# Performance work log

Hardware: AMD Instinct MI355X
Metric: run time of the kernel (lower is better)

The kernel has to match this reference:

```python
import jax, jax.numpy as jnp
import numpy as np

D_MODEL = 768
N_HEADS = 4
HEAD_DIM = D_MODEL // N_HEADS


def setup_inputs() -> dict:
    key = jax.random.key(0)
    ks = jax.random.split(key, 9)
    B, S = 4, 2048
    scale = 1.0 / np.sqrt(D_MODEL)
    inputs = jax.random.normal(ks[0], (B, S, D_MODEL), dtype=jnp.float32)
    # Linear weights stored as [in, out] for x @ W + b
    Wq = jax.random.normal(ks[1], (D_MODEL, D_MODEL), dtype=jnp.float32) * scale
    bq = jnp.zeros((D_MODEL,), dtype=jnp.float32)
    Wk = jax.random.normal(ks[2], (D_MODEL, D_MODEL), dtype=jnp.float32) * scale
    bk = jnp.zeros((D_MODEL,), dtype=jnp.float32)
    Wv = jax.random.normal(ks[3], (D_MODEL, D_MODEL), dtype=jnp.float32) * scale
    bv = jnp.zeros((D_MODEL,), dtype=jnp.float32)
    Wo = jax.random.normal(ks[4], (D_MODEL, D_MODEL), dtype=jnp.float32) * scale
    bo = jnp.zeros((D_MODEL,), dtype=jnp.float32)
    return {"inputs": inputs, "Wq": Wq, "bq": bq, "Wk": Wk, "bk": bk,
            "Wv": Wv, "bv": bv, "Wo": Wo, "bo": bo}


def reference(inputs, Wq, bq, Wk, bk, Wv, bv, Wo, bo):
    B, S, _ = inputs.shape
    H, Dh = N_HEADS, HEAD_DIM
    # projections -> [B, H, S, Dh]
    def split_heads(x):
        return x.reshape(B, S, H, Dh).transpose(0, 2, 1, 3)
    Q = split_heads(inputs @ Wq + bq)
    K = split_heads(inputs @ Wk + bk)
    V = split_heads(inputs @ Wv + bv)
    scores = jnp.einsum('bhqd,bhkd->bhqk', Q, K) / jnp.sqrt(jnp.float32(Dh))
    causal = jnp.tril(jnp.ones((S, S), dtype=bool))  # True = keep
    scores = jnp.where(causal, scores, -jnp.inf)
    weights = jax.nn.softmax(scores, axis=-1)
    # dropout is identity in eval mode
    ctx = jnp.einsum('bhqk,bhkd->bhqd', weights, V)
    ctx = ctx.transpose(0, 2, 1, 3).reshape(B, S, H * Dh)
    return ctx @ Wo + bo
```

## Files before the change

### kernel.cpp

```cpp
#include <hip/hip_runtime.h>
#include <hip/hip_bf16.h>
#include <cstddef>

typedef __attribute__((ext_vector_type(8))) short short8;
typedef __attribute__((ext_vector_type(4))) float f32x4;
typedef __attribute__((ext_vector_type(16))) float f32x16;
typedef __attribute__((ext_vector_type(4))) unsigned short u16x4;

#define D_MODEL 768
#define N_HEADS 4
#define HEAD_DIM 192
#define BATCH 4
#define SEQ 2048
#define M_ROWS (BATCH*SEQ)
#define QSCALE 0.10411754f

__device__ __forceinline__ short f2bf(float f) {
  union { float f; unsigned u; } v; v.f = f;
  unsigned r = v.u + 0x7FFFu + ((v.u >> 16) & 1u);
  return (short)(r >> 16);
}

__device__ __forceinline__ float fexp2(float x) {
  return __builtin_amdgcn_exp2f(x);
}

__device__ __forceinline__ void gl_lds16(const void* g, void* l) {
  __builtin_amdgcn_global_load_lds(
      (const __attribute__((address_space(1))) void*)g,
      (__attribute__((address_space(3))) void*)l, 16, 0, 0);
}

__global__ __launch_bounds__(256) void cast_kernel(const float* __restrict__ src,
                                                   short* __restrict__ dst, int n8) {
  int i = blockIdx.x * 256 + threadIdx.x;
  if (i >= n8) return;
  const float4* s = (const float4*)src;
  float4 a = s[2 * i], b = s[2 * i + 1];
  short8 o;
  o[0] = f2bf(a.x); o[1] = f2bf(a.y); o[2] = f2bf(a.z); o[3] = f2bf(a.w);
  o[4] = f2bf(b.x); o[5] = f2bf(b.y); o[6] = f2bf(b.z); o[7] = f2bf(b.w);
  *(short8*)(dst + (size_t)i * 8) = o;
}

__global__ __launch_bounds__(256) void wtrans4(const float* __restrict__ W0,
                                               const float* __restrict__ W1,
                                               const float* __restrict__ W2,
                                               const float* __restrict__ W3,
                                               short* __restrict__ Wqkvt,
                                               short* __restrict__ Wot) {
  __shared__ float tile[32][33];
  int z = blockIdx.z;
  const float* W = z == 0 ? W0 : (z == 1 ? W1 : (z == 2 ? W2 : W3));
  short* Wt = z < 3 ? (Wqkvt + (size_t)z * 768 * 768) : Wot;
  int k0 = blockIdx.x * 32, n0 = blockIdx.y * 32;
  int tc = threadIdx.x & 31, tr = threadIdx.x >> 5;
#pragma unroll
  for (int i = 0; i < 4; i++)
    tile[tr + i * 8][tc] = W[(size_t)(k0 + tr + i * 8) * D_MODEL + n0 + tc];
  __syncthreads();
#pragma unroll
  for (int i = 0; i < 4; i++)
    Wt[(size_t)(n0 + tr + i * 8) * D_MODEL + k0 + tc] = f2bf(tile[tc][tr + i * 8]);
}

template <int MODE>
__global__ __launch_bounds__(256, 4) void gemm_bf16(const short* __restrict__ A,
                                                    const short* __restrict__ Wt,
                                                    const float* __restrict__ b0,
                                                    const float* __restrict__ b1,
                                                    const float* __restrict__ b2,
                                                    short* __restrict__ oQ,
                                                    short* __restrict__ oK,
                                                    short* __restrict__ oV,
                                                    float* __restrict__ oF,
                                                    int N, int NB) {
  __shared__ short As[128 * 64];
  __shared__ short Bs[128 * 64];
  const int K = 768;
  const int lid = blockIdx.x;
  const int nlid = (lid & 7) * ((int)gridDim.x >> 3) + (lid >> 3);
  const int m0 = (nlid / NB) * 128, n0 = (nlid % NB) * 128;
  const int t = threadIdx.x, lane = t & 63, w = t >> 6;
  const int wr = w >> 1, wc = w & 1, lr = lane & 15, lg = lane >> 4;

  f32x4 acc[4][4] = {};

  for (int k0 = 0; k0 < K; k0 += 64) {
#pragma unroll
    for (int i = 0; i < 4; i++) {
      int id = w * 4 + i;
      int row = id * 8 + (lane >> 3);
      int cc = (lane & 7) ^ (row & 7);
      gl_lds16(A + (size_t)(m0 + row) * K + k0 + cc * 8, As + id * 512);
      gl_lds16(Wt + (size_t)(n0 + row) * K + k0 + cc * 8, Bs + id * 512);
    }
    __syncthreads();
#pragma unroll
    for (int kb = 0; kb < 2; kb++) {
      short8 a[4], b[4];
#pragma unroll
      for (int m = 0; m < 4; m++) {
        int row = wr * 64 + m * 16 + lr;
        a[m] = *(const short8*)&As[row * 64 + (((kb * 4 + lg) ^ (row & 7)) << 3)];
      }
#pragma unroll
      for (int n = 0; n < 4; n++) {
        int row = wc * 64 + n * 16 + lr;
        b[n] = *(const short8*)&Bs[row * 64 + (((kb * 4 + lg) ^ (row & 7)) << 3)];
      }
#pragma unroll
      for (int m = 0; m < 4; m++)
#pragma unroll
        for (int n = 0; n < 4; n++)
          acc[m][n] = __builtin_amdgcn_mfma_f32_16x16x32_bf16(a[m], b[n], acc[m][n], 0, 0, 0);
    }
    __syncthreads();
  }

  if (MODE == 0) {
#pragma unroll
    for (int m = 0; m < 4; m++)
#pragma unroll
      for (int n = 0; n < 4; n++) {
        int col = n0 + wc * 64 + n * 16 + lr;
        float bv = b0[col];
#pragma unroll
        for (int r = 0; r < 4; r++) {
          int row = m0 + wr * 64 + m * 16 + lg * 4 + r;
          oF[(size_t)row * N + col] = acc[m][n][r] + bv;
        }
      }
  } else {
    const int bb = m0 >> 11;
#pragma unroll
    for (int m = 0; m < 4; m++) {
      int s0 = (m0 & (SEQ - 1)) + wr * 64 + m * 16 + lg * 4;
#pragma unroll
      for (int n = 0; n < 4; n++) {
        int col = n0 + wc * 64 + n * 16 + lr;
        int seg = col / 768;
        int d = col - seg * 768;
        int h = d / HEAD_DIM, dd = d - h * HEAD_DIM;
        int bh = bb * N_HEADS + h;
        float bv = (seg == 0 ? b0 : (seg == 1 ? b1 : b2))[d];
        if (seg < 2) {
          short* dst = seg == 0 ? oQ : oK;
          float qs = seg == 0 ? QSCALE : 1.0f;
#pragma unroll
          for (int r = 0; r < 4; r++)
            dst[((size_t)bh * SEQ + s0 + r) * HEAD_DIM + dd] = f2bf((acc[m][n][r] + bv) * qs);
        } else {
          u16x4 pk;
#pragma unroll
          for (int r = 0; r < 4; r++) pk[r] = (unsigned short)f2bf(acc[m][n][r] + bv);
          *(u16x4*)&oV[((size_t)bh * HEAD_DIM + dd) * SEQ + s0] = pk;
        }
      }
    }
  }
}

__device__ __forceinline__ void stage_kv(const short* Kp, const short* Vp, int kbase,
                                         short* KsB, short* VsB, int w, int lane) {
#pragma unroll
  for (int i = 0; i < 6; i++) {
    int id = w * 6 + i;
    int o16 = id * 64 + lane;
    int row = o16 / 24, cc0 = o16 - row * 24;
    int cc = cc0 ^ (row & 7);
    gl_lds16(Kp + (size_t)(kbase + row) * HEAD_DIM + cc * 8, KsB + id * 512);
  }
#pragma unroll
  for (int i = 0; i < 6; i++) {
    int id = w * 6 + i;
    int o16 = id * 64 + lane;
    int row = o16 >> 3, cc = (o16 & 7) ^ (row & 7);
    gl_lds16(Vp + (size_t)row * SEQ + kbase + cc * 8, VsB + id * 512);
  }
}

__global__ __launch_bounds__(256, 2) void attn_kernel(const short* __restrict__ Q,
                                                      const short* __restrict__ Kg,
                                                      const short* __restrict__ Vt,
                                                      short* __restrict__ ctx) {
  __shared__ short smem[64 * 192 + 192 * 64];
  __shared__ float mlbuf[128];
  short* Ks = smem;
  short* Vs = smem + 64 * 192;
  float* obuf = (float*)smem;

  const int i = blockIdx.x;
  int bh, qt;
  if (i < 256) { bh = i & 15; qt = 31 - (i >> 4); }
  else         { int j = i - 256; bh = j & 15; qt = j >> 4; }

  const int b = bh >> 2, head = bh & 3;
  const short* Qp = Q + (size_t)bh * SEQ * HEAD_DIM;
  const short* Kp = Kg + (size_t)bh * SEQ * HEAD_DIM;
  const short* Vp = Vt + (size_t)bh * HEAD_DIM * SEQ;
  const int t = threadIdx.x, lane = t & 63, w = t >> 6;
  const int wq = w >> 1, wk = w & 1;
  const int l31 = lane & 31, hl = lane >> 5;

  const int nkb = qt + 1;
  const int q0w = qt * 64 + wq * 32;
  const int qlane = q0w + l31;

  short8 qf[12];
#pragma unroll
  for (int c = 0; c < 12; c++)
    qf[c] = *(const short8*)&Qp[(size_t)qlane * HEAD_DIM + c * 16 + hl * 8];

  f32x16 oacc[6];
#pragma unroll
  for (int d = 0; d < 6; d++) oacc[d] = 0.f;
  float m = -3.0e38f, lsum = 0.f;

  for (int kb = 0; kb < nkb; kb++) {
    const int kbase = kb * 64;
    stage_kv(Kp, Vp, kbase, Ks, Vs, w, lane);
    asm volatile("s_waitcnt vmcnt(0)" ::: "memory");
    __builtin_amdgcn_s_barrier();
    asm volatile("" ::: "memory");

    if (kbase + wk * 32 <= q0w + 31) {
      f32x16 sacc = 0.f, sacc2 = 0.f;
      const int krow = wk * 32 + l31;
      const int krb = krow * 192;
      const int kswz = (krow & 7) << 3;
      __builtin_amdgcn_s_setprio(1);
#pragma unroll
      for (int c = 0; c < 12; c += 2) {
        short8 kf0 = *(const short8*)&Ks[krb + ((c * 16 + hl * 8) ^ kswz)];
        short8 kf1 = *(const short8*)&Ks[krb + (((c + 1) * 16 + hl * 8) ^ kswz)];
        sacc = __builtin_amdgcn_mfma_f32_32x32x16_bf16(kf0, qf[c], sacc, 0, 0, 0);
        sacc2 = __builtin_amdgcn_mfma_f32_32x32x16_bf16(kf1, qf[c + 1], sacc2, 0, 0, 0);
      }
      __builtin_amdgcn_s_setprio(0);

      float sv[16];
      const bool need_mask = (kbase + wk * 32 + 31) > q0w;
      const int kb0 = kbase + wk * 32 + 4 * hl;
#pragma unroll
      for (int r = 0; r < 16; r++) {
        float v = sacc[r] + sacc2[r];
        if (need_mask) {
          int kg = kb0 + (r & 3) + 8 * (r >> 2);
          if (kg > qlane) v = -3.0e38f;
        }
        sv[r] = v;
      }
      float ma = fmaxf(fmaxf(sv[0], sv[1]), fmaxf(sv[2], sv[3]));
      float mb = fmaxf(fmaxf(sv[4], sv[5]), fmaxf(sv[6], sv[7]));
      float mc = fmaxf(fmaxf(sv[8], sv[9]), fmaxf(sv[10], sv[11]));
      float md = fmaxf(fmaxf(sv[12], sv[13]), fmaxf(sv[14], sv[15]));
      float mx = fmaxf(fmaxf(ma, mb), fmaxf(mc, md));
      mx = fmaxf(mx, __shfl_xor(mx, 32, 64));
      if (!__all(mx <= m + 8.0f)) {
        float mn = fmaxf(m, mx);
        float al = fexp2(m - mn);
        m = mn;
        lsum *= al;
#pragma unroll
        for (int d = 0; d < 6; d++) oacc[d] *= al;
      }
      float pr[16];
#pragma unroll
      for (int r = 0; r < 16; r++) pr[r] = fexp2(sv[r] - m);
      float sa = (pr[0] + pr[1]) + (pr[2] + pr[3]);
      float sb = (pr[4] + pr[5]) + (pr[6] + pr[7]);
      float sc = (pr[8] + pr[9]) + (pr[10] + pr[11]);
      float sd = (pr[12] + pr[13]) + (pr[14] + pr[15]);
      float rs = (sa + sb) + (sc + sd);
      rs += __shfl_xor(rs, 32, 64);
      lsum += rs;

      unsigned pk[8], ex[8];
#pragma unroll
      for (int j = 0; j < 8; j++) {
        unsigned r0;
        asm("v_cvt_pk_bf16_f32 %0, %1, %2" : "=v"(r0) : "v"(pr[2 * j]), "v"(pr[2 * j + 1]));
        pk[j] = r0;
      }
#pragma unroll
      for (int j = 0; j < 8; j++) ex[j] = __shfl_xor((int)pk[j], 32, 64);
      union { unsigned u[4]; short8 s8; } f0, f1;
      f0.u[0] = hl ? ex[2] : pk[0];
      f0.u[1] = hl ? ex[3] : pk[1];
      f0.u[2] = hl ? pk[2] : ex[0];
      f0.u[3] = hl ? pk[3] : ex[1];
      f1.u[0] = hl ? ex[6] : pk[4];
      f1.u[1] = hl ? ex[7] : pk[5];
      f1.u[2] = hl ? pk[6] : ex[4];
      f1.u[3] = hl ? pk[7] : ex[5];

      __builtin_amdgcn_s_setprio(1);
#pragma unroll
      for (int db = 0; db < 6; db++) {
        const int vrow = db * 32 + l31;
        const int vrb = vrow * 64;
        const int vswz = (vrow & 7) << 3;
        short8 va = *(const short8*)&Vs[vrb + ((wk * 32 + hl * 8) ^ vswz)];
        oacc[db] = __builtin_amdgcn_mfma_f32_32x32x16_bf16(va, f0.s8, oacc[db], 0, 0, 0);
        short8 vb = *(const short8*)&Vs[vrb + ((wk * 32 + 16 + hl * 8) ^ vswz)];
        oacc[db] = __builtin_amdgcn_mfma_f32_32x32x16_bf16(vb, f1.s8, oacc[db], 0, 0, 0);
      }
      __builtin_amdgcn_s_setprio(0);
    }
    asm volatile("" ::: "memory");
    __builtin_amdgcn_s_barrier();
  }

  __syncthreads();
  if (wk == 1) {
    if (lane < 32) {
      mlbuf[wq * 64 + lane] = m;
      mlbuf[wq * 64 + 32 + lane] = lsum;
    }
#pragma unroll
    for (int db = 0; db < 6; db++)
#pragma unroll
      for (int g = 0; g < 4; g++) {
        int d = db * 32 + 8 * g + 4 * hl;
        f32x4 vv;
        vv[0] = oacc[db][4 * g];
        vv[1] = oacc[db][4 * g + 1];
        vv[2] = oacc[db][4 * g + 2];
        vv[3] = oacc[db][4 * g + 3];
        *(f32x4*)&obuf[(wq * 32 + l31) * 192 + (d ^ ((l31 & 7) << 2))] = vv;
      }
  }
  __syncthreads();
  if (wk == 0) {
    float m1 = mlbuf[wq * 64 + l31];
    float l1 = mlbuf[wq * 64 + 32 + l31];
    float ms = fmaxf(m, m1);
    float a0 = fexp2(m - ms), a1 = fexp2(m1 - ms);
    float lt = lsum * a0 + l1 * a1;
    float rl = 1.0f / lt;
#pragma unroll
    for (int db = 0; db < 6; db++)
#pragma unroll
      for (int g = 0; g < 4; g++) {
        int d = db * 32 + 8 * g + 4 * hl;
        f32x4 rd = *(const f32x4*)&obuf[(wq * 32 + l31) * 192 + (d ^ ((l31 & 7) << 2))];
        u16x4 pkk;
#pragma unroll
        for (int r2 = 0; r2 < 4; r2++) {
          float v = (oacc[db][4 * g + r2] * a0 + rd[r2] * a1) * rl;
          pkk[r2] = (unsigned short)f2bf(v);
        }
        *(u16x4*)&ctx[((size_t)b * SEQ + qlane) * D_MODEL + head * HEAD_DIM + d] = pkk;
      }
  }
}

extern "C" void kernel_launch(void* const* d_in, const int* in_sizes, int n_in,
                              void* d_out, int out_size, void* d_ws, size_t ws_size,
                              hipStream_t stream) {
  const float* X  = (const float*)d_in[0];
  const float* Wq = (const float*)d_in[1];
  const float* bq = (const float*)d_in[2];
  const float* Wk = (const float*)d_in[3];
  const float* bk = (const float*)d_in[4];
  const float* Wv = (const float*)d_in[5];
  const float* bv = (const float*)d_in[6];
  const float* Wo = (const float*)d_in[7];
  const float* bo = (const float*)d_in[8];

  char* ws = (char*)d_ws;
  const size_t XB = (size_t)M_ROWS * D_MODEL * 2;
  const size_t WQKV = (size_t)3 * D_MODEL * D_MODEL * 2;
  const size_t WB = (size_t)D_MODEL * D_MODEL * 2;

  short* Xb    = (short*)(ws);
  short* Wqkvt = (short*)(ws + XB);
  short* Wot   = (short*)(ws + XB + WQKV);
  short* Qb    = (short*)(ws + XB + WQKV + WB + 12288);
  short* Kb    = (short*)(ws + XB + WQKV + WB + 12288 + XB);
  short* Vtb   = (short*)(ws + XB + WQKV + WB + 12288 + 2 * XB);
  short* Cb    = (short*)(ws + XB + WQKV + WB + 12288 + 3 * XB);

  const int n8x = M_ROWS * D_MODEL / 8;
  cast_kernel<<<(n8x + 255) / 256, 256, 0, stream>>>(X, Xb, n8x);
  wtrans4<<<dim3(24, 24, 4), 256, 0, stream>>>(Wq, Wk, Wv, Wo, Wqkvt, Wot);

  gemm_bf16<1><<<1152, 256, 0, stream>>>(Xb, Wqkvt, bq, bk, bv,
                                         Qb, Kb, Vtb, nullptr, 2304, 18);

  attn_kernel<<<512, 256, 0, stream>>>(Qb, Kb, Vtb, Cb);

  gemm_bf16<0><<<384, 256, 0, stream>>>(Cb, Wot, bo, bo, bo,
                                        nullptr, nullptr, nullptr, (float*)d_out, 768, 6);
}
```

Before: 141.5 us.

## Split causal attention KV range across two blocks and merge partials in separate kernel

Attention now uses 128-row query tiles with each warp owning 32 query rows, and splits each tile's KV range into two halves handled by separate blocks. Each block writes fp32 partial outputs plus max and sum to workspace, and a new merge kernel combines them into bf16 context. This replaces the old in-block split of key columns across warps, which needed an LDS reduction and did redundant Q loads. The aim is better load balance and more K/V reuse per stage. The cost is an extra kernel launch and about 50 MB of fp32 partial traffic through global memory.

```diff
diff --git a/kernel.cpp b/kernel.cpp
--- a/kernel.cpp
+++ b/kernel.cpp
@@ -183,28 +183,27 @@
 __global__ __launch_bounds__(256, 2) void attn_kernel(const short* __restrict__ Q,
                                                       const short* __restrict__ Kg,
                                                       const short* __restrict__ Vt,
-                                                      short* __restrict__ ctx) {
+                                                      float* __restrict__ Pbuf,
+                                                      float* __restrict__ Mbuf) {
   __shared__ short smem[64 * 192 + 192 * 64];
-  __shared__ float mlbuf[128];
   short* Ks = smem;
   short* Vs = smem + 64 * 192;
-  float* obuf = (float*)smem;
 
   const int i = blockIdx.x;
-  int bh, qt;
-  if (i < 256) { bh = i & 15; qt = 31 - (i >> 4); }
-  else         { int j = i - 256; bh = j & 15; qt = j >> 4; }
-
-  const int b = bh >> 2, head = bh & 3;
+  int bh, j, h;
+  if (i < 256) { bh = i & 15; j = i >> 4;        h = 0; }
+  else         { int p = i - 256; bh = p & 15; j = 15 - (p >> 4); h = 1; }
+  const int u0 = h == 0 ? 0 : j + 1;
+  const int u1 = h == 0 ? j + 1 : 2 * j + 2;
+  const int sidx = (bh * 16 + j) * 2 + h;
+
   const short* Qp = Q + (size_t)bh * SEQ * HEAD_DIM;
   const short* Kp = Kg + (size_t)bh * SEQ * HEAD_DIM;
   const short* Vp = Vt + (size_t)bh * HEAD_DIM * SEQ;
   const int t = threadIdx.x, lane = t & 63, w = t >> 6;
-  const int wq = w >> 1, wk = w & 1;
   const int l31 = lane & 31, hl = lane >> 5;
 
-  const int nkb = qt + 1;
-  const int q0w = qt * 64 + wq * 32;
+  const int q0w = j * 128 + w * 32;
   const int qlane = q0w + l31;
 
   short8 qf[12];
@@ -217,142 +216,151 @@
   for (int d = 0; d < 6; d++) oacc[d] = 0.f;
   float m = -3.0e38f, lsum = 0.f;
 
-  for (int kb = 0; kb < nkb; kb++) {
-    const int kbase = kb * 64;
+  for (int u = u0; u < u1; u++) {
+    const int kbase = u * 64;
     stage_kv(Kp, Vp, kbase, Ks, Vs, w, lane);
     asm volatile("s_waitcnt vmcnt(0)" ::: "memory");
     __builtin_amdgcn_s_barrier();
     asm volatile("" ::: "memory");
 
-    if (kbase + wk * 32 <= q0w + 31) {
-      f32x16 sacc = 0.f, sacc2 = 0.f;
-      const int krow = wk * 32 + l31;
-      const int krb = krow * 192;
-      const int kswz = (krow & 7) << 3;
-      __builtin_amdgcn_s_setprio(1);
-#pragma unroll
-      for (int c = 0; c < 12; c += 2) {
-        short8 kf0 = *(const short8*)&Ks[krb + ((c * 16 + hl * 8) ^ kswz)];
-        short8 kf1 = *(const short8*)&Ks[krb + (((c + 1) * 16 + hl * 8) ^ kswz)];
-        sacc = __builtin_amdgcn_mfma_f32_32x32x16_bf16(kf0, qf[c], sacc, 0, 0, 0);
-        sacc2 = __builtin_amdgcn_mfma_f32_32x32x16_bf16(kf1, qf[c + 1], sacc2, 0, 0, 0);
+#pragma unroll
+    for (int kc = 0; kc < 2; kc++) {
+      if (kbase + kc * 32 <= q0w + 31) {
+        f32x16 sacc = 0.f, sacc2 = 0.f;
+        const int krow = kc * 32 + l31;
+        const int krb = krow * 192;
+        const int kswz = (krow & 7) << 3;
+        __builtin_amdgcn_s_setprio(1);
+#pragma unroll
+        for (int c = 0; c < 12; c += 2) {
+          short8 kf0 = *(const short8*)&Ks[krb + ((c * 16 + hl * 8) ^ kswz)];
+          short8 kf1 = *(const short8*)&Ks[krb + (((c + 1) * 16 + hl * 8) ^ kswz)];
+          sacc = __builtin_amdgcn_mfma_f32_32x32x16_bf16(kf0, qf[c], sacc, 0, 0, 0);
+          sacc2 = __builtin_amdgcn_mfma_f32_32x32x16_bf16(kf1, qf[c + 1], sacc2, 0, 0, 0);
+        }
+        __builtin_amdgcn_s_setprio(0);
+
+        float sv[16];
+        const bool need_mask = (kbase + kc * 32 + 31) > q0w;
+        const int kb0 = kbase + kc * 32 + 4 * hl;
+#pragma unroll
+        for (int r = 0; r < 16; r++) {
+          float v = sacc[r] + sacc2[r];
+          if (need_mask) {
+            int kg = kb0 + (r & 3) + 8 * (r >> 2);
+            if (kg > qlane) v = -3.0e38f;
+          }
+          sv[r] = v;
+        }
+        float ma = fmaxf(fmaxf(sv[0], sv[1]), fmaxf(sv[2], sv[3]));
+        float mb = fmaxf(fmaxf(sv[4], sv[5]), fmaxf(sv[6], sv[7]));
+        float mc = fmaxf(fmaxf(sv[8], sv[9]), fmaxf(sv[10], sv[11]));
+        float md = fmaxf(fmaxf(sv[12], sv[13]), fmaxf(sv[14], sv[15]));
+        float mx = fmaxf(fmaxf(ma, mb), fmaxf(mc, md));
+        mx = fmaxf(mx, __shfl_xor(mx, 32, 64));
+        if (!__all(mx <= m + 8.0f)) {
+          float mn = fmaxf(m, mx);
+          float al = fexp2(m - mn);
+          m = mn;
+          lsum *= al;
+#pragma unroll
+          for (int d = 0; d < 6; d++) oacc[d] *= al;
+        }
+        float pr[16];
+#pragma unroll
+        for (int r = 0; r < 16; r++) pr[r] = fexp2(sv[r] - m);
+        float sa = (pr[0] + pr[1]) + (pr[2] + pr[3]);
+        float sb = (pr[4] + pr[5]) + (pr[6] + pr[7]);
+        float sc = (pr[8] + pr[9]) + (pr[10] + pr[11]);
+        float sd = (pr[12] + pr[13]) + (pr[14] + pr[15]);
+        float rs = (sa + sb) + (sc + sd);
+        rs += __shfl_xor(rs, 32, 64);
+        lsum += rs;
+
+        unsigned pk[8], ex[8];
+#pragma unroll
+        for (int jj = 0; jj < 8; jj++) {
+          unsigned r0;
+          asm("v_cvt_pk_bf16_f32 %0, %1, %2" : "=v"(r0) : "v"(pr[2 * jj]), "v"(pr[2 * jj + 1]));
+          pk[jj] = r0;
+        }
+#pragma unroll
+        for (int jj = 0; jj < 8; jj++) ex[jj] = __shfl_xor((int)pk[jj], 32, 64);
+        union { unsigned u4[4]; short8 s8; } f0, f1;
+        f0.u4[0] = hl ? ex[2] : pk[0];
+        f0.u4[1] = hl ? ex[3] : pk[1];
+        f0.u4[2] = hl ? pk[2] : ex[0];
+        f0.u4[3] = hl ? pk[3] : ex[1];
+        f1.u4[0] = hl ? ex[6] : pk[4];
+        f1.u4[1] = hl ? ex[7] : pk[5];
+        f1.u4[2] = hl ? pk[6] : ex[4];
+        f1.u4[3] = hl ? pk[7] : ex[5];
+
+        const int colA = kc * 32;
+        __builtin_amdgcn_s_setprio(1);
+#pragma unroll
+        for (int db = 0; db < 6; db++) {
+          const int vrow = db * 32 + l31;
+          const int vrb = vrow * 64;
+          const int vswz = (vrow & 7) << 3;
+          short8 va = *(const short8*)&Vs[vrb + ((colA + hl * 8) ^ vswz)];
+          oacc[db] = __builtin_amdgcn_mfma_f32_32x32x16_bf16(va, f0.s8, oacc[db], 0, 0, 0);
+          short8 vb = *(const short8*)&Vs[vrb + ((colA + 16 + hl * 8) ^ vswz)];
+          oacc[db] = __builtin_amdgcn_mfma_f32_32x32x16_bf16(vb, f1.s8, oacc[db], 0, 0, 0);
+        }
+        __builtin_amdgcn_s_setprio(0);
       }
-      __builtin_amdgcn_s_setprio(0);
-
-      float sv[16];
-      const bool need_mask = (kbase + wk * 32 + 31) > q0w;
-      const int kb0 = kbase + wk * 32 + 4 * hl;
-#pragma unroll
-      for (int r = 0; r < 16; r++) {
-        float v = sacc[r] + sacc2[r];
-        if (need_mask) {
-          int kg = kb0 + (r & 3) + 8 * (r >> 2);
-          if (kg > qlane) v = -3.0e38f;
-        }
-        sv[r] = v;
-      }
-      float ma = fmaxf(fmaxf(sv[0], sv[1]), fmaxf(sv[2], sv[3]));
-      float mb = fmaxf(fmaxf(sv[4], sv[5]), fmaxf(sv[6], sv[7]));
-      float mc = fmaxf(fmaxf(sv[8], sv[9]), fmaxf(sv[10], sv[11]));
-      float md = fmaxf(fmaxf(sv[12], sv[13]), fmaxf(sv[14], sv[15]));
-      float mx = fmaxf(fmaxf(ma, mb), fmaxf(mc, md));
-      mx = fmaxf(mx, __shfl_xor(mx, 32, 64));
-      if (!__all(mx <= m + 8.0f)) {
-        float mn = fmaxf(m, mx);
-        float al = fexp2(m - mn);
-        m = mn;
-        lsum *= al;
-#pragma unroll
-        for (int d = 0; d < 6; d++) oacc[d] *= al;
-      }
-      float pr[16];
-#pragma unroll
-      for (int r = 0; r < 16; r++) pr[r] = fexp2(sv[r] - m);
-      float sa = (pr[0] + pr[1]) + (pr[2] + pr[3]);
-      float sb = (pr[4] + pr[5]) + (pr[6] + pr[7]);
-      float sc = (pr[8] + pr[9]) + (pr[10] + pr[11]);
-      float sd = (pr[12] + pr[13]) + (pr[14] + pr[15]);
-      float rs = (sa + sb) + (sc + sd);
-      rs += __shfl_xor(rs, 32, 64);
-      lsum += rs;
-
-      unsigned pk[8], ex[8];
-#pragma unroll
-      for (int j = 0; j < 8; j++) {
-        unsigned r0;
-        asm("v_cvt_pk_bf16_f32 %0, %1, %2" : "=v"(r0) : "v"(pr[2 * j]), "v"(pr[2 * j + 1]));
-        pk[j] = r0;
-      }
-#pragma unroll
-      for (int j = 0; j < 8; j++) ex[j] = __shfl_xor((int)pk[j], 32, 64);
-      union { unsigned u[4]; short8 s8; } f0, f1;
-      f0.u[0] = hl ? ex[2] : pk[0];
-      f0.u[1] = hl ? ex[3] : pk[1];
-      f0.u[2] = hl ? pk[2] : ex[0];
-      f0.u[3] = hl ? pk[3] : ex[1];
-      f1.u[0] = hl ? ex[6] : pk[4];
-      f1.u[1] = hl ? ex[7] : pk[5];
-      f1.u[2] = hl ? pk[6] : ex[4];
-      f1.u[3] = hl ? pk[7] : ex[5];
-
-      __builtin_amdgcn_s_setprio(1);
-#pragma unroll
-      for (int db = 0; db < 6; db++) {
-        const int vrow = db * 32 + l31;
-        const int vrb = vrow * 64;
-        const int vswz = (vrow & 7) << 3;
-        short8 va = *(const short8*)&Vs[vrb + ((wk * 32 + hl * 8) ^ vswz)];
-        oacc[db] = __builtin_amdgcn_mfma_f32_32x32x16_bf16(va, f0.s8, oacc[db], 0, 0, 0);
-        short8 vb = *(const short8*)&Vs[vrb + ((wk * 32 + 16 + hl * 8) ^ vswz)];
-        oacc[db] = __builtin_amdgcn_mfma_f32_32x32x16_bf16(vb, f1.s8, oacc[db], 0, 0, 0);
-      }
-      __builtin_amdgcn_s_setprio(0);
     }
     asm volatile("" ::: "memory");
     __builtin_amdgcn_s_barrier();
   }
 
-  __syncthreads();
-  if (wk == 1) {
-    if (lane < 32) {
-      mlbuf[wq * 64 + lane] = m;
-      mlbuf[wq * 64 + 32 + lane] = lsum;
+  const int row = w * 32 + l31;
+  float* Pb = Pbuf + (size_t)sidx * 128 * 192;
+  float* Mb = Mbuf + (size_t)sidx * 256;
+  if (hl == 0) { Mb[row] = m; Mb[128 + row] = lsum; }
+#pragma unroll
+  for (int db = 0; db < 6; db++)
+#pragma unroll
+    for (int g = 0; g < 4; g++) {
+      int d = db * 32 + 8 * g + 4 * hl;
+      f32x4 vv;
+      vv[0] = oacc[db][4 * g];
+      vv[1] = oacc[db][4 * g + 1];
+      vv[2] = oacc[db][4 * g + 2];
+      vv[3] = oacc[db][4 * g + 3];
+      *(f32x4*)&Pb[(size_t)row * 192 + d] = vv;
     }
-#pragma unroll
-    for (int db = 0; db < 6; db++)
-#pragma unroll
-      for (int g = 0; g < 4; g++) {
-        int d = db * 32 + 8 * g + 4 * hl;
-        f32x4 vv;
-        vv[0] = oacc[db][4 * g];
-        vv[1] = oacc[db][4 * g + 1];
-        vv[2] = oacc[db][4 * g + 2];
-        vv[3] = oacc[db][4 * g + 3];
-        *(f32x4*)&obuf[(wq * 32 + l31) * 192 + (d ^ ((l31 & 7) << 2))] = vv;
-      }
-  }
-  __syncthreads();
-  if (wk == 0) {
-    float m1 = mlbuf[wq * 64 + l31];
-    float l1 = mlbuf[wq * 64 + 32 + l31];
-    float ms = fmaxf(m, m1);
-    float a0 = fexp2(m - ms), a1 = fexp2(m1 - ms);
-    float lt = lsum * a0 + l1 * a1;
-    float rl = 1.0f / lt;
-#pragma unroll
-    for (int db = 0; db < 6; db++)
-#pragma unroll
-      for (int g = 0; g < 4; g++) {
-        int d = db * 32 + 8 * g + 4 * hl;
-        f32x4 rd = *(const f32x4*)&obuf[(wq * 32 + l31) * 192 + (d ^ ((l31 & 7) << 2))];
-        u16x4 pkk;
-#pragma unroll
-        for (int r2 = 0; r2 < 4; r2++) {
-          float v = (oacc[db][4 * g + r2] * a0 + rd[r2] * a1) * rl;
-          pkk[r2] = (unsigned short)f2bf(v);
-        }
-        *(u16x4*)&ctx[((size_t)b * SEQ + qlane) * D_MODEL + head * HEAD_DIM + d] = pkk;
-      }
+}
+
+__global__ __launch_bounds__(256) void attn_merge(const float* __restrict__ Pbuf,
+                                                  const float* __restrict__ Mbuf,
+                                                  short* __restrict__ ctx) {
+  const int blk = blockIdx.x;
+  const int bh = blk >> 4, j = blk & 15;
+  const int b = bh >> 2, head = bh & 3;
+  const int base = (bh * 16 + j) * 2;
+  const float* M0 = Mbuf + (size_t)base * 256;
+  const float* M1 = M0 + 256;
+  const float* P0 = Pbuf + (size_t)base * 128 * 192;
+  const float* P1 = P0 + 128 * 192;
+  const int t = threadIdx.x;
+  const int row = t & 127, cg = t >> 7;
+  float m0 = M0[row], l0 = M0[128 + row];
+  float m1 = M1[row], l1 = M1[128 + row];
+  float ms = fmaxf(m0, m1);
+  float a0 = fexp2(m0 - ms), a1 = fexp2(m1 - ms);
+  float rl = 1.0f / (l0 * a0 + l1 * a1);
+  const int q = j * 128 + row;
+#pragma unroll
+  for (int jj = 0; jj < 24; jj++) {
+    int d = cg * 96 + jj * 4;
+    f32x4 v0 = *(const f32x4*)&P0[(size_t)row * 192 + d];
+    f32x4 v1 = *(const f32x4*)&P1[(size_t)row * 192 + d];
+    u16x4 o;
+#pragma unroll
+    for (int r = 0; r < 4; r++) o[r] = (unsigned short)f2bf((v0[r] * a0 + v1[r] * a1) * rl);
+    *(u16x4*)&ctx[((size_t)b * SEQ + q) * D_MODEL + head * HEAD_DIM + d] = o;
   }
 }
 
@@ -381,6 +389,9 @@
   short* Kb    = (short*)(ws + XB + WQKV + WB + 12288 + XB);
   short* Vtb   = (short*)(ws + XB + WQKV + WB + 12288 + 2 * XB);
   short* Cb    = (short*)(ws + XB + WQKV + WB + 12288 + 3 * XB);
+  float* Pbuf  = (float*)(ws + XB + WQKV + WB + 12288 + 4 * XB);
+  float* Mbuf  = (float*)(ws + XB + WQKV + WB + 12288 + 4 * XB +
+                          (size_t)512 * 128 * 192 * 4);
 
   const int n8x = M_ROWS * D_MODEL / 8;
   cast_kernel<<<(n8x + 255) / 256, 256, 0, stream>>>(X, Xb, n8x);
@@ -389,7 +400,8 @@
   gemm_bf16<1><<<1152, 256, 0, stream>>>(Xb, Wqkvt, bq, bk, bv,
                                          Qb, Kb, Vtb, nullptr, 2304, 18);
 
-  attn_kernel<<<512, 256, 0, stream>>>(Qb, Kb, Vtb, Cb);
+  attn_kernel<<<512, 256, 0, stream>>>(Qb, Kb, Vtb, Pbuf, Mbuf);
+  attn_merge<<<256, 256, 0, stream>>>(Pbuf, Mbuf, Cb);
 
   gemm_bf16<0><<<384, 256, 0, stream>>>(Cb, Wot, bo, bo, bo,
                                         nullptr, nullptr, nullptr, (float*)d_out, 768, 6);
```

Measured after the change: 154.6 us. 9.2% more time.
